# Optimization experiments

Hardware: AMD Instinct MI355X
Metric: run time of the kernel (lower is better)

## Reference

```python
import jax, jax.numpy as jnp
import numpy as np
import math

EPS = 1e-7
K_NEIGHBORS = 32  # matches init kwarg k

def _project(x, c):
    norm = jnp.linalg.norm(x, axis=-1, keepdims=True).clip(EPS)
    sqrt_c = jnp.sqrt(c).clip(EPS)
    max_norm = (1.0 - EPS) / sqrt_c
    return x * jnp.minimum(max_norm / norm, 1.0)

def _mobius_add(x, y, c):
    x2 = jnp.sum(x * x, axis=-1, keepdims=True)
    y2 = jnp.sum(y * y, axis=-1, keepdims=True)
    xy = jnp.sum(x * y, axis=-1, keepdims=True)
    num = (1 + 2 * c * xy + c * y2) * x + (1 - c * x2) * y
    den = 1 + 2 * c * xy + c * c * x2 * y2
    return _project(num / den.clip(EPS), c)

def _dist(x, y, c):
    sqrt_c = jnp.sqrt(c).clip(EPS)
    diff = _mobius_add(x, -y, c)
    dn = jnp.linalg.norm(diff, axis=-1)
    arg = jnp.minimum(sqrt_c * dn.clip(EPS, 1 - EPS), 1.0 - EPS)
    return 2.0 * jnp.arctanh(arg) / sqrt_c

def _logmap0(y, c):
    sqrt_c = jnp.sqrt(c).clip(EPS)
    yn = jnp.linalg.norm(y, axis=-1, keepdims=True)
    is_zero = yn < EPS
    syn = yn.clip(EPS)
    arg = jnp.minimum(sqrt_c * syn, 1.0 - EPS)
    mag = jnp.arctanh(arg) / sqrt_c
    return jnp.where(is_zero, jnp.zeros_like(y), mag * y / syn)

def _layernorm(x, g, b):
    m = x.mean(-1, keepdims=True)
    v = x.var(-1, keepdims=True)
    return (x - m) / jnp.sqrt(v + 1e-6) * g + b

def setup_inputs() -> dict:
    key = jax.random.key(0)
    B, N, D, P, H = 2, 2048, 512, 3, 8
    ks = jax.random.split(key, 16)
    s = 0.02
    d = {}
    d['x'] = jax.random.normal(ks[0], (B, N, D), dtype=jnp.float32)
    d['positions'] = jax.random.normal(ks[1], (B, N, P), dtype=jnp.float32) * 0.1
    d['c'] = jnp.float32(1.0)
    d['Wq'] = jax.random.normal(ks[2], (D, D), jnp.float32) * s; d['bq'] = jnp.zeros((D,), jnp.float32)
    d['Wk'] = jax.random.normal(ks[3], (D, D), jnp.float32) * s; d['bk'] = jnp.zeros((D,), jnp.float32)
    d['Wv'] = jax.random.normal(ks[4], (D, D), jnp.float32) * s; d['bv'] = jnp.zeros((D,), jnp.float32)
    d['Wg'] = jax.random.normal(ks[5], (P, D), jnp.float32) * s; d['bg'] = jnp.zeros((D,), jnp.float32)
    d['Wo'] = jax.random.normal(ks[6], (D, D), jnp.float32) * s; d['bo'] = jnp.zeros((D,), jnp.float32)
    d['Wf1'] = jax.random.normal(ks[7], (D, 4 * D), jnp.float32) * s; d['bf1'] = jnp.zeros((4 * D,), jnp.float32)
    d['Wf2'] = jax.random.normal(ks[8], (4 * D, D), jnp.float32) * s; d['bf2'] = jnp.zeros((D,), jnp.float32)
    d['g1'] = jnp.ones((D,), jnp.float32); d['b1'] = jnp.zeros((D,), jnp.float32)
    d['g2'] = jnp.ones((D,), jnp.float32); d['b2'] = jnp.zeros((D,), jnp.float32)
    d['ascale'] = jnp.ones((H,), jnp.float32)
    d['fscale'] = jnp.ones((H,), jnp.float32)
    return d

def reference(x, positions, c, Wq, bq, Wk, bk, Wv, bv, Wg, bg, Wo, bo, Wf1, bf1, Wf2, bf2, g1, b1, g2, b2, ascale, fscale):
    B, N, D = x.shape
    H = ascale.shape[0]
    hd = D // H
    K = K_NEIGHBORS

    xn = _layernorm(x, g1, b1)
    q = (xn @ Wq + bq).reshape(B, N, H, hd)
    k = (xn @ Wk + bk).reshape(B, N, H, hd)
    v = (xn @ Wv + bv).reshape(B, N, H, hd)

    # full pairwise hyperbolic distance matrix [B, N, N]
    dmat = _dist(positions[:, :, None, :], positions[:, None, :, :], c)
    idx = jax.lax.top_k(-dmat, K)[1]  # [B, N, K]

    bidx = jnp.arange(B)[:, None, None]
    key_pos = positions[bidx, idx]                 # [B, N, K, P]
    qpos = positions[:, :, None, :]                # [B, N, 1, P]
    geo = _logmap0(_mobius_add(-qpos, key_pos, c), c)
    geo_v = (geo @ Wg + bg).reshape(B, N, K, H, hd)

    kg = k[bidx, idx]                              # [B, N, K, H, hd]
    vg = v[bidx, idx]

    align = jnp.einsum('bnhd,bnkhd->bhnk', q, geo_v)
    feat = jnp.einsum('bnhd,bnkhd->bhnk', q, kg) / math.sqrt(hd)
    scores = fscale[None, :, None, None] * feat + ascale[None, :, None, None] * align
    w = jax.nn.softmax(scores.astype(jnp.float32), axis=-1)
    attn = jnp.einsum('bhnk,bnkhd->bnhd', w, vg).reshape(B, N, D)

    x1 = x + attn @ Wo + bo
    h = _layernorm(x1, g2, b2)
    x2 = x1 + jax.nn.gelu(h @ Wf1 + bf1) @ Wf2 + bf2
    return x2
```

## Files before the change

kernel.cpp:

```cpp
#include <hip/hip_runtime.h>
#include <math.h>

#define EPSF 1e-7f

constexpr int Bb = 2, Nn = 2048, Dd = 512, Hh = 8, HD = 64, KK = 32;
constexpr int ROWS = Bb * Nn;

typedef __attribute__((ext_vector_type(8))) short bf16x8;
typedef __attribute__((ext_vector_type(4))) float f32x4;
typedef __attribute__((ext_vector_type(8))) unsigned short u16x8;
typedef unsigned long long u64;

__device__ inline unsigned short f2bf(float f) {
    union { float f; unsigned int u; } v; v.f = f;
    unsigned int u = v.u;
    unsigned int r = (u + 0x7fffu + ((u >> 16) & 1u)) >> 16;
    return (unsigned short)r;
}

__device__ inline float bf2f(short s) {
    union { unsigned int u; float f; } x;
    x.u = ((unsigned int)(unsigned short)s) << 16;
    return x.f;
}

__device__ inline float gelu_tanh(float v) {
    float u = v + 0.044715f * v * v * v;
    return 0.5f * v * (1.f + tanhf(0.79788456080286535588f * u));
}

__device__ __forceinline__ void tcvt(float (*tile)[65], const float* __restrict__ in,
                                     unsigned short* __restrict__ out,
                                     int K, int N, int bx, int by) {
    int k0 = by * 64, n0 = bx * 64;
    int t = threadIdx.x;
    int lr = t >> 6, lc = t & 63;
#pragma unroll 4
    for (int p = 0; p < 16; ++p) {
        int r = p * 4 + lr;
        tile[r][lc] = in[(size_t)(k0 + r) * N + n0 + lc];
    }
    __syncthreads();
#pragma unroll 4
    for (int p = 0; p < 16; ++p) {
        int n = p * 4 + lr;
        out[(size_t)(n0 + n) * K + k0 + lc] = f2bf(tile[lc][n]);
    }
}

__device__ __forceinline__ void ln_row(const float* __restrict__ x,
                                       const float* __restrict__ g,
                                       const float* __restrict__ b,
                                       unsigned short* __restrict__ out,
                                       int row, int lane) {
    const float* xr = x + (size_t)row * Dd;
    float4 v0 = *(const float4*)(xr + lane * 8);
    float4 v1 = *(const float4*)(xr + lane * 8 + 4);
    float s = v0.x + v0.y + v0.z + v0.w + v1.x + v1.y + v1.z + v1.w;
    float s2 = v0.x * v0.x + v0.y * v0.y + v0.z * v0.z + v0.w * v0.w +
               v1.x * v1.x + v1.y * v1.y + v1.z * v1.z + v1.w * v1.w;
    for (int o = 32; o; o >>= 1) { s += __shfl_xor(s, o); s2 += __shfl_xor(s2, o); }
    float mean = s * (1.f / Dd);
    float var = s2 * (1.f / Dd) - mean * mean;
    float rstd = rsqrtf(var + 1e-6f);
    float4 g0 = *(const float4*)(g + lane * 8);
    float4 g1v = *(const float4*)(g + lane * 8 + 4);
    float4 b0 = *(const float4*)(b + lane * 8);
    float4 b1v = *(const float4*)(b + lane * 8 + 4);
    u16x8 o;
    o[0] = f2bf((v0.x - mean) * rstd * g0.x + b0.x);
    o[1] = f2bf((v0.y - mean) * rstd * g0.y + b0.y);
    o[2] = f2bf((v0.z - mean) * rstd * g0.z + b0.z);
    o[3] = f2bf((v0.w - mean) * rstd * g0.w + b0.w);
    o[4] = f2bf((v1.x - mean) * rstd * g1v.x + b1v.x);
    o[5] = f2bf((v1.y - mean) * rstd * g1v.y + b1v.y);
    o[6] = f2bf((v1.z - mean) * rstd * g1v.z + b1v.z);
    o[7] = f2bf((v1.w - mean) * rstd * g1v.w + b1v.w);
    *(u16x8*)(out + (size_t)row * Dd + lane * 8) = o;
}

__global__ __launch_bounds__(256) void ln_kernel(const float* __restrict__ x,
                                                 const float* __restrict__ g,
                                                 const float* __restrict__ b,
                                                 unsigned short* __restrict__ out) {
    ln_row(x, g, b, out, blockIdx.x * 4 + (threadIdx.x >> 6), threadIdx.x & 63);
}

__global__ __launch_bounds__(256) void prep_kernel(
    const float* __restrict__ Wq, const float* __restrict__ Wk,
    const float* __restrict__ Wv, const float* __restrict__ Wo,
    const float* __restrict__ Wf1, const float* __restrict__ Wf2,
    const float* __restrict__ bq, const float* __restrict__ bk, const float* __restrict__ bv,
    const float* __restrict__ x, const float* __restrict__ g1, const float* __restrict__ b1,
    unsigned short* __restrict__ wqkv_t, unsigned short* __restrict__ wo_t,
    unsigned short* __restrict__ wf1_t, unsigned short* __restrict__ wf2_t,
    float* __restrict__ bqkv, unsigned short* __restrict__ xn) {
    __shared__ float tile[64][65];
    int bid = blockIdx.x;
    if (bid < 256) {
        int z = bid >> 6, r = bid & 63;
        const float* in = (z == 0) ? Wq : (z == 1) ? Wk : (z == 2) ? Wv : Wo;
        unsigned short* out = (z == 0) ? wqkv_t : (z == 1) ? wqkv_t + 262144
                            : (z == 2) ? wqkv_t + 524288 : wo_t;
        tcvt(tile, in, out, 512, 512, r & 7, r >> 3);
    } else if (bid < 512) {
        int r = bid - 256;
        tcvt(tile, Wf1, wf1_t, 512, 2048, r & 31, r >> 5);
    } else if (bid < 768) {
        int r = bid - 512;
        tcvt(tile, Wf2, wf2_t, 2048, 512, r & 7, r >> 3);
    } else if (bid < 774) {
        int t = (bid - 768) * 256 + threadIdx.x;
        if (t < 512) bqkv[t] = bq[t];
        else if (t < 1024) bqkv[t] = bk[t - 512];
        else if (t < 1536) bqkv[t] = bv[t - 1024];
    } else {
        ln_row(x, g1, b1, xn, (bid - 774) * 4 + (threadIdx.x >> 6), threadIdx.x & 63);
    }
}

template <int EPI, int OBF16>
__device__ __forceinline__ void gemm64_body(short* __restrict__ As, short* __restrict__ Bs,
                                            const unsigned short* __restrict__ A,
                                            const unsigned short* __restrict__ Bt,
                                            const float* __restrict__ bias,
                                            const float* __restrict__ resid,
                                            void* __restrict__ C,
                                            int N, int K, int gridX, int nwg, int wgid) {
    int cpx = nwg >> 3;
    int nid = (wgid & 7) * cpx + (wgid >> 3);
    int bx = nid % gridX, by = nid / gridX;
    int bm = by * 64, bn = bx * 64;
    int tid = threadIdx.x;
    int wave = tid >> 6, lane = tid & 63;
    int wr = wave >> 1, wc = wave & 1;
    f32x4 acc[2][2] = {};

    int srow = wave * 8 + (lane >> 3);
    int scol = ((lane & 7) ^ (lane >> 3)) * 8;
    const unsigned short* gA0 = A + (size_t)(bm + srow) * K + scol;
    const unsigned short* gA1 = A + (size_t)(bm + srow + 32) * K + scol;
    const unsigned short* gB0 = Bt + (size_t)(bn + srow) * K + scol;
    const unsigned short* gB1 = Bt + (size_t)(bn + srow + 32) * K + scol;

#define STAGE(buf, kof)                                                                                 \
    do {                                                                                                \
        __builtin_amdgcn_global_load_lds((const __attribute__((address_space(1))) void*)(gA0 + (kof)), \
            (__attribute__((address_space(3))) void*)(As + (buf) * 4096 + wave * 512), 16, 0, 0);       \
        __builtin_amdgcn_global_load_lds((const __attribute__((address_space(1))) void*)(gA1 + (kof)), \
            (__attribute__((address_space(3))) void*)(As + (buf) * 4096 + 2048 + wave * 512), 16, 0, 0);\
        __builtin_amdgcn_global_load_lds((const __attribute__((address_space(1))) void*)(gB0 + (kof)), \
            (__attribute__((address_space(3))) void*)(Bs + (buf) * 4096 + wave * 512), 16, 0, 0);       \
        __builtin_amdgcn_global_load_lds((const __attribute__((address_space(1))) void*)(gB1 + (kof)), \
            (__attribute__((address_space(3))) void*)(Bs + (buf) * 4096 + 2048 + wave * 512), 16, 0, 0);\
    } while (0)

    int nt = K >> 6;
    int cur = 0;
    STAGE(0, 0);
    __syncthreads();
    for (int t = 0; t < nt; ++t) {
        if (t + 1 < nt) STAGE(cur ^ 1, (t + 1) * 64);
        const short* as = As + cur * 4096;
        const short* bs = Bs + cur * 4096;
#pragma unroll
        for (int kk = 0; kk < 64; kk += 32) {
            int kx = (kk + (lane >> 4) * 8) ^ ((lane & 7) << 3);
            bf16x8 a0 = *(const bf16x8*)(as + (wr * 32 + (lane & 15)) * 64 + kx);
            bf16x8 a1 = *(const bf16x8*)(as + (wr * 32 + 16 + (lane & 15)) * 64 + kx);
            bf16x8 b0 = *(const bf16x8*)(bs + (wc * 32 + (lane & 15)) * 64 + kx);
            bf16x8 b1 = *(const bf16x8*)(bs + (wc * 32 + 16 + (lane & 15)) * 64 + kx);
            acc[0][0] = __builtin_amdgcn_mfma_f32_16x16x32_bf16(a0, b0, acc[0][0], 0, 0, 0);
            acc[0][1] = __builtin_amdgcn_mfma_f32_16x16x32_bf16(a0, b1, acc[0][1], 0, 0, 0);
            acc[1][0] = __builtin_amdgcn_mfma_f32_16x16x32_bf16(a1, b0, acc[1][0], 0, 0, 0);
            acc[1][1] = __builtin_amdgcn_mfma_f32_16x16x32_bf16(a1, b1, acc[1][1], 0, 0, 0);
        }
        __syncthreads();
        cur ^= 1;
    }
#undef STAGE

    int cbase = bn + wc * 32 + (lane & 15);
    int rbase = bm + wr * 32 + (lane >> 4) * 4;
    float bias_v[2] = {bias[cbase], bias[cbase + 16]};
#pragma unroll
    for (int mi = 0; mi < 2; ++mi) {
#pragma unroll
        for (int r = 0; r < 4; ++r) {
            int row = rbase + mi * 16 + r;
#pragma unroll
            for (int ni = 0; ni < 2; ++ni) {
                int col = cbase + ni * 16;
                float v = acc[mi][ni][r] + bias_v[ni];
                if (EPI == 1) v += resid[(size_t)row * N + col];
                if (EPI == 2) v = gelu_tanh(v);
                if (OBF16) ((unsigned short*)C)[(size_t)row * N + col] = f2bf(v);
                else ((float*)C)[(size_t)row * N + col] = v;
            }
        }
    }
}

template <int EPI, int OBF16>
__global__ __launch_bounds__(256) void gemm64(const unsigned short* __restrict__ A,
                                              const unsigned short* __restrict__ Bt,
                                              const float* __restrict__ bias,
                                              const float* __restrict__ resid,
                                              void* __restrict__ C,
                                              int N, int K, int gridX) {
    __shared__ short As[2 * 64 * 64];
    __shared__ short Bs[2 * 64 * 64];
    gemm64_body<EPI, OBF16>(As, Bs, A, Bt, bias, resid, C, N, K, gridX, gridDim.x, blockIdx.x);
}

template <int CTRL>
__device__ inline u64 dpp_u64(u64 v) {
    int lo = (int)(unsigned int)v;
    int hi = (int)(unsigned int)(v >> 32);
    lo = __builtin_amdgcn_update_dpp(lo, lo, CTRL, 0xF, 0xF, false);
    hi = __builtin_amdgcn_update_dpp(hi, hi, CTRL, 0xF, 0xF, false);
    return ((u64)(unsigned int)hi << 32) | (unsigned int)lo;
}

__device__ inline u64 wave_min_u64(u64 v) {
    u64 o;
    o = dpp_u64<0xB1>(v);  if (o < v) v = o;
    o = dpp_u64<0x4E>(v);  if (o < v) v = o;
    o = dpp_u64<0x141>(v); if (o < v) v = o;
    o = dpp_u64<0x140>(v); if (o < v) v = o;
    o = __shfl_xor(v, 16); if (o < v) v = o;
    o = __shfl_xor(v, 32); if (o < v) v = o;
    return v;
}

__device__ __forceinline__ void topk_body(char* smem, const float* __restrict__ pos,
                                          const float* __restrict__ cp,
                                          int* __restrict__ idx_out, int bid) {
    float* s_px = (float*)smem;
    float* s_py = s_px + Nn;
    float* s_pz = s_py + Nn;
    float* s_u  = s_pz + Nn;
    int* s_out  = (int*)(s_u + Nn);
    int b = bid >> 9;
    int q0 = (bid & 511) * 4;
    int t = threadIdx.x;
    float c = *cp;
    const float* pb = pos + (size_t)b * Nn * 3;
    for (int j = t; j < Nn; j += 256) {
        float px = pb[j * 3 + 0], py = pb[j * 3 + 1], pz = pb[j * 3 + 2];
        s_px[j] = px; s_py[j] = py; s_pz[j] = pz;
        s_u[j] = c * (px * px + py * py + pz * pz);
    }
    __syncthreads();
    int wave = t >> 6, lane = t & 63;
    int n = q0 + wave;
    float qx = s_px[n], qy = s_py[n], qz = s_pz[n];
    float cx2 = s_u[n];
    float x2 = cx2 / c;
    float B = 1.f - cx2;
    float rc = 1.f / c;
    float B2rc = B * B * rc;
    float m2c = -2.f * c;
    float m2B = -2.f * B;
    float key[32];
#pragma unroll
    for (int i = 0; i < 32; ++i) {
        int j = i * 64 + lane;
        float dot = qx * s_px[j] + qy * s_py[j] + qz * s_pz[j];
        float su = s_u[j];
        float r = fmaf(m2c, dot, 1.f);
        float A = r + su;
        float den = fmaf(cx2, su, r);
        float p1 = x2 * A;
        float q1 = A * dot;
        float t1 = fmaf(m2B, q1, B2rc * su);
        float num2 = fmaf(p1, A, t1);
        float rd = __builtin_amdgcn_rcpf(den);
        key[i] = num2 * rd * rd;
    }
    const u64 MAXK = ~0ull;
    u64 B0 = MAXK, B1 = MAXK, B2 = MAXK, B3 = MAXK;
#pragma unroll
    for (int i = 0; i < 32; ++i) {
        u64 k = ((u64)__float_as_uint(key[i]) << 32) | (unsigned int)(i * 64 + lane);
        if (k < B3) {
            B3 = k;
            if (B3 < B2) { u64 tmp = B2; B2 = B3; B3 = tmp; }
            if (B2 < B1) { u64 tmp = B1; B1 = B2; B2 = tmp; }
            if (B1 < B0) { u64 tmp = B0; B0 = B1; B1 = tmp; }
        }
    }
    int bcount = 4, consumed = 0;
    u64 last = 0;
    for (int s2 = 0; s2 < KK; ++s2) {
        bool need = (bcount == 0) && (consumed < 32);
        if (__any(need)) {
            if (need) {
                B0 = MAXK; B1 = MAXK; B2 = MAXK; B3 = MAXK;
#pragma unroll
                for (int i = 0; i < 32; ++i) {
                    u64 k = ((u64)__float_as_uint(key[i]) << 32) | (unsigned int)(i * 64 + lane);
                    if (k > last && k < B3) {
                        B3 = k;
                        if (B3 < B2) { u64 tmp = B2; B2 = B3; B3 = tmp; }
                        if (B2 < B1) { u64 tmp = B1; B1 = B2; B2 = tmp; }
                        if (B1 < B0) { u64 tmp = B0; B0 = B1; B1 = tmp; }
                    }
                }
                int rem = 32 - consumed;
                bcount = rem < 4 ? rem : 4;
            }
        }
        u64 offer = (bcount > 0) ? B0 : MAXK;
        u64 g = wave_min_u64(offer);
        if (lane == 0) s_out[wave * KK + s2] = (int)(unsigned int)g;
        if (offer == g) {
            B0 = B1; B1 = B2; B2 = B3; B3 = MAXK;
            --bcount; ++consumed; last = g;
        }
    }
    if (lane < KK) idx_out[(size_t)(b * Nn + n) * KK + lane] = s_out[wave * KK + lane];
}

__global__ __launch_bounds__(256) void qkv_topk_kernel(const unsigned short* __restrict__ A,
                                                       const unsigned short* __restrict__ Wqkv,
                                                       const float* __restrict__ bqkv,
                                                       unsigned short* __restrict__ qkv,
                                                       const float* __restrict__ pos,
                                                       const float* __restrict__ cp,
                                                       int* __restrict__ idx_out) {
    __shared__ __align__(16) char smem[33280];
    if (blockIdx.x < 1536) {
        short* As = (short*)smem;
        short* Bs = (short*)(smem + 16384);
        gemm64_body<0, 1>(As, Bs, A, Wqkv, bqkv, nullptr, qkv, 1536, 512, 24, 1536, blockIdx.x);
    } else {
        topk_body(smem, pos, cp, idx_out, blockIdx.x - 1536);
    }
}

__global__ __launch_bounds__(256) void attn_kernel(const unsigned short* __restrict__ qkv,
                                                   const int* __restrict__ idx,
                                                   const float* __restrict__ pos,
                                                   const float* __restrict__ Wg,
                                                   const float* __restrict__ bg,
                                                   const float* __restrict__ ascale,
                                                   const float* __restrict__ fscale,
                                                   const float* __restrict__ cp,
                                                   unsigned short* __restrict__ out) {
    constexpr int QS = 1536;
    int bid = blockIdx.x;
    int xcd = bid & 7, slot = bid >> 3;
    int b = xcd >> 2;
    int n = (xcd & 3) * 512 + slot;
    int bn = b * Nn + n;
    int t = threadIdx.x;
    int wave = t >> 6, lane = t & 63;
    __shared__ float s_q[Dd];
    __shared__ float s_geo[KK][3];
    __shared__ int s_idx[KK];
    __shared__ float s_qg[Hh][3];
    __shared__ float s_qb[Hh];
    __shared__ float s_dot[KK][9];
    __shared__ float s_w[Hh][KK];
    __shared__ float s_part[4][Dd];
    float c = *cp;
    if (t >= 64 && t < 96) s_idx[t - 64] = idx[(size_t)bn * KK + (t - 64)];
    if (t < 64) {
        bf16x8 q8 = *(const bf16x8*)(qkv + (size_t)bn * QS + t * 8);
#pragma unroll
        for (int j = 0; j < 8; ++j) s_q[t * 8 + j] = bf2f(q8[j]);
    }
    __syncthreads();
    if (t < KK) {
        const float* qp = pos + (size_t)bn * 3;
        const float* kp = pos + (size_t)(b * Nn + s_idx[t]) * 3;
        float xx = -qp[0], xyc = -qp[1], xz = -qp[2];
        float yx = kp[0], yy = kp[1], yz = kp[2];
        float x2 = xx * xx + xyc * xyc + xz * xz;
        float y2 = yx * yx + yy * yy + yz * yz;
        float xy = xx * yx + xyc * yy + xz * yz;
        float Av = 1.f + 2.f * c * xy + c * y2;
        float Bv = 1.f - c * x2;
        float den = fmaxf(1.f + 2.f * c * xy + c * c * x2 * y2, EPSF);
        float mx = (Av * xx + Bv * yx) / den;
        float my = (Av * xyc + Bv * yy) / den;
        float mz = (Av * xz + Bv * yz) / den;
        float rn = fmaxf(sqrtf(mx * mx + my * my + mz * mz), EPSF);
        float sqrt_c = fmaxf(sqrtf(c), EPSF);
        float max_norm = (1.f - EPSF) / sqrt_c;
        float scpr = fminf(max_norm / rn, 1.f);
        mx *= scpr; my *= scpr; mz *= scpr;
        float yn = sqrtf(mx * mx + my * my + mz * mz);
        if (yn < EPSF) {
            s_geo[t][0] = 0.f; s_geo[t][1] = 0.f; s_geo[t][2] = 0.f;
        } else {
            float syn = fmaxf(yn, EPSF);
            float arg = fminf(sqrt_c * syn, 1.f - EPSF);
            float mag = atanhf(arg) / sqrt_c;
            float f = mag / syn;
            s_geo[t][0] = mx * f; s_geo[t][1] = my * f; s_geo[t][2] = mz * f;
        }
    } else if (t >= 64 && t < 88) {
        int h = (t - 64) / 3, p = (t - 64) % 3;
        float acc = 0.f;
        for (int d2 = 0; d2 < HD; ++d2) acc += s_q[h * HD + d2] * Wg[p * Dd + h * HD + d2];
        s_qg[h][p] = acc;
    } else if (t >= 96 && t < 104) {
        int h = t - 96;
        float acc = 0.f;
        for (int d2 = 0; d2 < HD; ++d2) acc += s_q[h * HD + d2] * bg[h * HD + d2];
        s_qb[h] = acc;
    }
    {
#pragma unroll
        for (int r = 0; r < 8; ++r) {
            int kk = wave * 8 + r;
            int nk = s_idx[kk];
            bf16x8 k8 = *(const bf16x8*)(qkv + (size_t)(b * Nn + nk) * QS + 512 + lane * 8);
            float p = 0.f;
#pragma unroll
            for (int j = 0; j < 8; ++j) p = fmaf(bf2f(k8[j]), s_q[lane * 8 + j], p);
            p += __shfl_xor(p, 1);
            p += __shfl_xor(p, 2);
            p += __shfl_xor(p, 4);
            if ((lane & 7) == 0) s_dot[kk][lane >> 3] = p;
        }
    }
    __syncthreads();
    {
        int h = t >> 5, kk = t & 31;
        float align = s_geo[kk][0] * s_qg[h][0] + s_geo[kk][1] * s_qg[h][1] +
                      s_geo[kk][2] * s_qg[h][2] + s_qb[h];
        float scv = fscale[h] * s_dot[kk][h] * 0.125f + ascale[h] * align;
        float m = scv;
        for (int o = 16; o; o >>= 1) m = fmaxf(m, __shfl_xor(m, o));
        float e = expf(scv - m);
        float ss = e;
        for (int o = 16; o; o >>= 1) ss += __shfl_xor(ss, o);
        s_w[h][kk] = e / ss;
    }
    __syncthreads();
    {
        float acc[8] = {0.f, 0.f, 0.f, 0.f, 0.f, 0.f, 0.f, 0.f};
        int h = lane >> 3;
#pragma unroll
        for (int r = 0; r < 8; ++r) {
            int kk = wave * 8 + r;
            int nk = s_idx[kk];
            bf16x8 v8 = *(const bf16x8*)(qkv + (size_t)(b * Nn + nk) * QS + 1024 + lane * 8);
            float wgt = s_w[h][kk];
#pragma unroll
            for (int j = 0; j < 8; ++j) acc[j] = fmaf(bf2f(v8[j]), wgt, acc[j]);
        }
#pragma unroll
        for (int j = 0; j < 8; ++j) s_part[wave][lane * 8 + j] = acc[j];
    }
    __syncthreads();
    for (int d = t; d < Dd; d += 256) {
        float s = s_part[0][d] + s_part[1][d] + s_part[2][d] + s_part[3][d];
        out[(size_t)bn * Dd + d] = f2bf(s);
    }
}

extern "C" void kernel_launch(void* const* d_in, const int* in_sizes, int n_in,
                              void* d_out, int out_size, void* d_ws, size_t ws_size,
                              hipStream_t stream) {
    const float* x   = (const float*)d_in[0];
    const float* pos = (const float*)d_in[1];
    const float* cp  = (const float*)d_in[2];
    const float* Wq  = (const float*)d_in[3];
    const float* bq  = (const float*)d_in[4];
    const float* Wk  = (const float*)d_in[5];
    const float* bk  = (const float*)d_in[6];
    const float* Wv  = (const float*)d_in[7];
    const float* bv  = (const float*)d_in[8];
    const float* Wg  = (const float*)d_in[9];
    const float* bg  = (const float*)d_in[10];
    const float* Wo  = (const float*)d_in[11];
    const float* bo  = (const float*)d_in[12];
    const float* Wf1 = (const float*)d_in[13];
    const float* bf1 = (const float*)d_in[14];
    const float* Wf2 = (const float*)d_in[15];
    const float* bf2 = (const float*)d_in[16];
    const float* g1  = (const float*)d_in[17];
    const float* b1  = (const float*)d_in[18];
    const float* g2  = (const float*)d_in[19];
    const float* b2  = (const float*)d_in[20];
    const float* asc = (const float*)d_in[21];
    const float* fsc = (const float*)d_in[22];
    float* out = (float*)d_out;
    char* ws = (char*)d_ws;

    unsigned short* qkv_bf  = (unsigned short*)(ws + 0);
    unsigned short* t_bf    = (unsigned short*)(ws + 0);
    unsigned short* xn_bf   = (unsigned short*)(ws + 25165824);
    float*          x1      = (float*)(ws + 29360128);
    unsigned short* attn_bf = (unsigned short*)(ws + 37748736);
    unsigned short* wqkv_t  = (unsigned short*)(ws + 41943040);
    unsigned short* wo_t    = (unsigned short*)(ws + 43515904);
    unsigned short* wf1_t   = (unsigned short*)(ws + 44040192);
    unsigned short* wf2_t   = (unsigned short*)(ws + 46137344);
    int*            idx     = (int*)(ws + 48234496);
    float*          bqkv    = (float*)(ws + 48758784);

    prep_kernel<<<1798, 256, 0, stream>>>(Wq, Wk, Wv, Wo, Wf1, Wf2, bq, bk, bv,
                                          x, g1, b1, wqkv_t, wo_t, wf1_t, wf2_t, bqkv, xn_bf);
    qkv_topk_kernel<<<2560, 256, 0, stream>>>(xn_bf, wqkv_t, bqkv, qkv_bf, pos, cp, idx);
    attn_kernel<<<ROWS, 256, 0, stream>>>(qkv_bf, idx, pos, Wg, bg, asc, fsc, cp, attn_bf);
    gemm64<1, 0><<<512, 256, 0, stream>>>(attn_bf, wo_t, bo, x, x1, 512, 512, 8);
    ln_kernel<<<ROWS / 4, 256, 0, stream>>>(x1, g2, b2, xn_bf);
    gemm64<2, 1><<<2048, 256, 0, stream>>>(xn_bf, wf1_t, bf1, nullptr, t_bf, 2048, 512, 32);
    gemm64<1, 0><<<512, 256, 0, stream>>>(t_bf, wf2_t, bf2, x1, out, 512, 2048, 8);
}
```

Measured before the change: 138.3 us.

## Add 128x128-tile GEMM for QKV and FFN1, split topk into own kernel

Adds a new gemm128 kernel in which each 256-thread block computes a 128x128 output tile (4x4 MFMA fragments per wave), and uses it for the QKV projection and the first FFN GEMM. The aim is more operand reuse per LDS load and fewer blocks. The previously fused qkv+topk launch is split into a standalone topk kernel with launch_bounds occupancy 3, followed by the QKV GEMM. The new GEMM is single-buffered, with a sync before and after each k-step, so load/compute overlap is lost and the larger accumulator raises register pressure.

```diff
diff --git a/kernel.cpp b/kernel.cpp
--- a/kernel.cpp
+++ b/kernel.cpp
@@ -120,14 +120,93 @@
 }
 
 template <int EPI, int OBF16>
-__device__ __forceinline__ void gemm64_body(short* __restrict__ As, short* __restrict__ Bs,
-                                            const unsigned short* __restrict__ A,
-                                            const unsigned short* __restrict__ Bt,
-                                            const float* __restrict__ bias,
-                                            const float* __restrict__ resid,
-                                            void* __restrict__ C,
-                                            int N, int K, int gridX, int nwg, int wgid) {
+__global__ __launch_bounds__(256) void gemm128(const unsigned short* __restrict__ A,
+                                               const unsigned short* __restrict__ Bt,
+                                               const float* __restrict__ bias,
+                                               const float* __restrict__ resid,
+                                               void* __restrict__ C,
+                                               int N, int K, int gridX) {
+    __shared__ short As[128 * 64];
+    __shared__ short Bs[128 * 64];
+    int nwg = gridDim.x;
     int cpx = nwg >> 3;
+    int wgid = blockIdx.x;
+    int nid = (wgid & 7) * cpx + (wgid >> 3);
+    int bx = nid % gridX, by = nid / gridX;
+    int bm = by * 128, bn = bx * 128;
+    int tid = threadIdx.x;
+    int wave = tid >> 6, lane = tid & 63;
+    int wr = wave >> 1, wc = wave & 1;
+    f32x4 acc[4][4] = {};
+
+    int scol = ((lane & 7) ^ (lane >> 3)) * 8;
+    for (int k0 = 0; k0 < K; k0 += 64) {
+#pragma unroll
+        for (int c2 = 0; c2 < 4; ++c2) {
+            int row = wave * 32 + c2 * 8 + (lane >> 3);
+            const unsigned short* ga = A + (size_t)(bm + row) * K + k0 + scol;
+            const unsigned short* gb = Bt + (size_t)(bn + row) * K + k0 + scol;
+            __builtin_amdgcn_global_load_lds(
+                (const __attribute__((address_space(1))) void*)ga,
+                (__attribute__((address_space(3))) void*)(As + wave * 2048 + c2 * 512), 16, 0, 0);
+            __builtin_amdgcn_global_load_lds(
+                (const __attribute__((address_space(1))) void*)gb,
+                (__attribute__((address_space(3))) void*)(Bs + wave * 2048 + c2 * 512), 16, 0, 0);
+        }
+        __syncthreads();
+#pragma unroll
+        for (int kk = 0; kk < 64; kk += 32) {
+            int kx = (kk + (lane >> 4) * 8) ^ ((lane & 7) << 3);
+            bf16x8 af[4], bfr[4];
+#pragma unroll
+            for (int mi = 0; mi < 4; ++mi)
+                af[mi] = *(const bf16x8*)(As + (wr * 64 + mi * 16 + (lane & 15)) * 64 + kx);
+#pragma unroll
+            for (int ni = 0; ni < 4; ++ni)
+                bfr[ni] = *(const bf16x8*)(Bs + (wc * 64 + ni * 16 + (lane & 15)) * 64 + kx);
+#pragma unroll
+            for (int mi = 0; mi < 4; ++mi)
+#pragma unroll
+                for (int ni = 0; ni < 4; ++ni)
+                    acc[mi][ni] = __builtin_amdgcn_mfma_f32_16x16x32_bf16(af[mi], bfr[ni], acc[mi][ni], 0, 0, 0);
+        }
+        __syncthreads();
+    }
+    int cbase = bn + wc * 64 + (lane & 15);
+    int rbase = bm + wr * 64 + (lane >> 4) * 4;
+    float bias_v[4];
+#pragma unroll
+    for (int ni = 0; ni < 4; ++ni) bias_v[ni] = bias[cbase + ni * 16];
+#pragma unroll
+    for (int mi = 0; mi < 4; ++mi) {
+#pragma unroll
+        for (int r = 0; r < 4; ++r) {
+            int row = rbase + mi * 16 + r;
+#pragma unroll
+            for (int ni = 0; ni < 4; ++ni) {
+                int col = cbase + ni * 16;
+                float v = acc[mi][ni][r] + bias_v[ni];
+                if (EPI == 1) v += resid[(size_t)row * N + col];
+                if (EPI == 2) v = gelu_tanh(v);
+                if (OBF16) ((unsigned short*)C)[(size_t)row * N + col] = f2bf(v);
+                else ((float*)C)[(size_t)row * N + col] = v;
+            }
+        }
+    }
+}
+
+template <int EPI, int OBF16>
+__global__ __launch_bounds__(256) void gemm64(const unsigned short* __restrict__ A,
+                                              const unsigned short* __restrict__ Bt,
+                                              const float* __restrict__ bias,
+                                              const float* __restrict__ resid,
+                                              void* __restrict__ C,
+                                              int N, int K, int gridX) {
+    __shared__ short As[2 * 64 * 64];
+    __shared__ short Bs[2 * 64 * 64];
+    int nwg = gridDim.x;
+    int cpx = nwg >> 3;
+    int wgid = blockIdx.x;
     int nid = (wgid & 7) * cpx + (wgid >> 3);
     int bx = nid % gridX, by = nid / gridX;
     int bm = by * 64, bn = bx * 64;
@@ -201,18 +280,6 @@
     }
 }
 
-template <int EPI, int OBF16>
-__global__ __launch_bounds__(256) void gemm64(const unsigned short* __restrict__ A,
-                                              const unsigned short* __restrict__ Bt,
-                                              const float* __restrict__ bias,
-                                              const float* __restrict__ resid,
-                                              void* __restrict__ C,
-                                              int N, int K, int gridX) {
-    __shared__ short As[2 * 64 * 64];
-    __shared__ short Bs[2 * 64 * 64];
-    gemm64_body<EPI, OBF16>(As, Bs, A, Bt, bias, resid, C, N, K, gridX, gridDim.x, blockIdx.x);
-}
-
 template <int CTRL>
 __device__ inline u64 dpp_u64(u64 v) {
     int lo = (int)(unsigned int)v;
@@ -233,16 +300,13 @@
     return v;
 }
 
-__device__ __forceinline__ void topk_body(char* smem, const float* __restrict__ pos,
-                                          const float* __restrict__ cp,
-                                          int* __restrict__ idx_out, int bid) {
-    float* s_px = (float*)smem;
-    float* s_py = s_px + Nn;
-    float* s_pz = s_py + Nn;
-    float* s_u  = s_pz + Nn;
-    int* s_out  = (int*)(s_u + Nn);
-    int b = bid >> 9;
-    int q0 = (bid & 511) * 4;
+__global__ __launch_bounds__(256, 3) void topk_kernel(const float* __restrict__ pos,
+                                                      const float* __restrict__ cp,
+                                                      int* __restrict__ idx_out) {
+    __shared__ float s_px[Nn], s_py[Nn], s_pz[Nn], s_u[Nn];
+    __shared__ int s_out[4][KK];
+    int b = blockIdx.x >> 9;
+    int q0 = (blockIdx.x & 511) * 4;
     int t = threadIdx.x;
     float c = *cp;
     const float* pb = pos + (size_t)b * Nn * 3;
@@ -313,30 +377,13 @@
         }
         u64 offer = (bcount > 0) ? B0 : MAXK;
         u64 g = wave_min_u64(offer);
-        if (lane == 0) s_out[wave * KK + s2] = (int)(unsigned int)g;
+        if (lane == 0) s_out[wave][s2] = (int)(unsigned int)g;
         if (offer == g) {
             B0 = B1; B1 = B2; B2 = B3; B3 = MAXK;
             --bcount; ++consumed; last = g;
         }
     }
-    if (lane < KK) idx_out[(size_t)(b * Nn + n) * KK + lane] = s_out[wave * KK + lane];
-}
-
-__global__ __launch_bounds__(256) void qkv_topk_kernel(const unsigned short* __restrict__ A,
-                                                       const unsigned short* __restrict__ Wqkv,
-                                                       const float* __restrict__ bqkv,
-                                                       unsigned short* __restrict__ qkv,
-                                                       const float* __restrict__ pos,
-                                                       const float* __restrict__ cp,
-                                                       int* __restrict__ idx_out) {
-    __shared__ __align__(16) char smem[33280];
-    if (blockIdx.x < 1536) {
-        short* As = (short*)smem;
-        short* Bs = (short*)(smem + 16384);
-        gemm64_body<0, 1>(As, Bs, A, Wqkv, bqkv, nullptr, qkv, 1536, 512, 24, 1536, blockIdx.x);
-    } else {
-        topk_body(smem, pos, cp, idx_out, blockIdx.x - 1536);
-    }
+    if (lane < KK) idx_out[(size_t)(b * Nn + n) * KK + lane] = s_out[wave][lane];
 }
 
 __global__ __launch_bounds__(256) void attn_kernel(const unsigned short* __restrict__ qkv,
@@ -506,10 +553,11 @@
 
     prep_kernel<<<1798, 256, 0, stream>>>(Wq, Wk, Wv, Wo, Wf1, Wf2, bq, bk, bv,
                                           x, g1, b1, wqkv_t, wo_t, wf1_t, wf2_t, bqkv, xn_bf);
-    qkv_topk_kernel<<<2560, 256, 0, stream>>>(xn_bf, wqkv_t, bqkv, qkv_bf, pos, cp, idx);
+    topk_kernel<<<ROWS / 4, 256, 0, stream>>>(pos, cp, idx);
+    gemm128<0, 1><<<384, 256, 0, stream>>>(xn_bf, wqkv_t, bqkv, nullptr, qkv_bf, 1536, 512, 12);
     attn_kernel<<<ROWS, 256, 0, stream>>>(qkv_bf, idx, pos, Wg, bg, asc, fsc, cp, attn_bf);
     gemm64<1, 0><<<512, 256, 0, stream>>>(attn_bf, wo_t, bo, x, x1, 512, 512, 8);
     ln_kernel<<<ROWS / 4, 256, 0, stream>>>(x1, g2, b2, xn_bf);
-    gemm64<2, 1><<<2048, 256, 0, stream>>>(xn_bf, wf1_t, bf1, nullptr, t_bf, 2048, 512, 32);
+    gemm128<2, 1><<<512, 256, 0, stream>>>(xn_bf, wf1_t, bf1, nullptr, t_bf, 2048, 512, 16);
     gemm64<1, 0><<<512, 256, 0, stream>>>(t_bf, wf2_t, bf2, x1, out, 512, 2048, 8);
 }
```

New measurement: 141.4 us. 2.2% more time.
